# Optimization experiments

Hardware: AMD Instinct MI355X
Metric: run time of the kernel (lower is better)

The kernel has to match this reference:

```python
import jax, jax.numpy as jnp
import numpy as np

DIM, WIDTH = 5, 64
BATCH, N_SAVE = 4096, 64
RTOL, ATOL = 1e-3, 1e-6
SAFETY, FMIN, FMAX = 0.9, 0.2, 10.0
MAX_STEPS, DT0, EPS = 64, 0.1, 1e-6

# Tsit5 (Tsitouras 2011) Butcher tableau
A21 = 0.161
A31, A32 = -0.008480655492356989, 0.335480655492357
A41, A42, A43 = 2.8971530571054935, -6.359448489975075, 4.3622954328695815
A51, A52, A53, A54 = 5.325864828439257, -11.748883564062828, 7.4955393428898365, -0.09249506636175525
A61, A62, A63, A64, A65 = 5.86145544294642, -12.92096931784711, 8.159367898576159, -0.071584973281401, -0.028269050394068383
B1, B2, B3, B4, B5, B6 = 0.09646076681806523, 0.01, 0.4798896504144996, 1.379008574103742, -3.290069515436081, 2.324710524099774
# embedded 4th-order error coefficients (b - bhat)
E1, E2, E3, E4, E5, E6, E7 = (-0.00178001105222577714, -0.0008164344596567469,
    0.007880878010261995, -0.1447110071732629, 0.5823571654525552,
    -0.45808210592918697, 0.015151515151515152)


def _mlp(y, W1, b1, W2, b2, W3, b3, W4, b4):
    # eqx.nn.MLP(5, 5, width 64, depth 3, softplus)
    h = jax.nn.softplus(y @ W1.T + b1)
    h = jax.nn.softplus(h @ W2.T + b2)
    h = jax.nn.softplus(h @ W3.T + b3)
    return h @ W4.T + b4


def _solve_one(y0, t_eval, params):
    f = lambda y: _mlp(y, *params)
    t0, t1 = t_eval[0], t_eval[-1]
    # save points at/before t0 get y0
    ys0 = jnp.where((t_eval <= t0 + EPS)[:, None], y0[None, :], 0.0)

    def body(carry, _):
        t, y, h, ys = carry
        done = t >= t1 - EPS
        hc = jnp.where(done, 0.0, jnp.minimum(h, t1 - t))  # clip last step to t1
        k1 = f(y)
        k2 = f(y + hc * (A21 * k1))
        k3 = f(y + hc * (A31 * k1 + A32 * k2))
        k4 = f(y + hc * (A41 * k1 + A42 * k2 + A43 * k3))
        k5 = f(y + hc * (A51 * k1 + A52 * k2 + A53 * k3 + A54 * k4))
        k6 = f(y + hc * (A61 * k1 + A62 * k2 + A63 * k3 + A64 * k4 + A65 * k5))
        ynew = y + hc * (B1 * k1 + B2 * k2 + B3 * k3 + B4 * k4 + B5 * k5 + B6 * k6)
        k7 = f(ynew)  # FSAL stage, also used for error + interpolation
        err = hc * (E1 * k1 + E2 * k2 + E3 * k3 + E4 * k4 + E5 * k5 + E6 * k6 + E7 * k7)
        scale = ATOL + RTOL * jnp.maximum(jnp.abs(y), jnp.abs(ynew))
        enorm = jnp.sqrt(jnp.mean((err / scale) ** 2))
        enorm_c = jax.lax.stop_gradient(jnp.maximum(enorm, 1e-10))
        accept = enorm <= 1.0
        factor = jnp.clip(SAFETY * enorm_c ** -0.2, FMIN, FMAX)  # I-controller, order 5
        step_ok = accept & ~done
        t_next = jnp.where(step_ok, t + hc, t)
        y_next = jnp.where(step_ok, ynew, y)
        h_next = jnp.where(done, h, hc * factor)
        # cubic Hermite interpolation for save points inside (t, t_next]
        s = ((t_eval - t) / jnp.maximum(hc, 1e-12))[:, None]
        h00 = 2 * s**3 - 3 * s**2 + 1
        h10 = s**3 - 2 * s**2 + s
        h01 = -2 * s**3 + 3 * s**2
        h11 = s**3 - s**2
        yi = h00 * y + h10 * hc * k1 + h01 * ynew + h11 * hc * k7
        mask = (t_eval > t) & (t_eval <= t_next + EPS) & step_ok
        ys = jnp.where(mask[:, None], yi, ys)
        return (t_next, y_next, h_next, ys), None

    h0 = jnp.asarray(DT0, dtype=y0.dtype)
    (_, _, _, ys), _ = jax.lax.scan(body, (t0, y0, h0, ys0), None, length=MAX_STEPS)
    return ys  # [N_SAVE, DIM]


def setup_inputs() -> dict:
    key = jax.random.key(0)
    ks = jax.random.split(key, 9)
    y0 = jax.random.normal(ks[0], (BATCH, DIM), dtype=jnp.float32)
    t_eval = jnp.linspace(0.0, 1.0, N_SAVE, dtype=jnp.float32)

    def lin(k, out_d, in_d):
        lim = 1.0 / np.sqrt(in_d)
        kw, kb = jax.random.split(k)
        W = jax.random.uniform(kw, (out_d, in_d), jnp.float32, -lim, lim)
        b = jax.random.uniform(kb, (out_d,), jnp.float32, -lim, lim)
        return W, b

    W1, b1 = lin(ks[1], WIDTH, DIM)
    W2, b2 = lin(ks[2], WIDTH, WIDTH)
    W3, b3 = lin(ks[3], WIDTH, WIDTH)
    W4, b4 = lin(ks[4], DIM, WIDTH)
    return {"y0": y0, "t_eval": t_eval, "W1": W1, "b1": b1, "W2": W2, "b2": b2,
            "W3": W3, "b3": b3, "W4": W4, "b4": b4}


def reference(y0, t_eval, W1, b1, W2, b2, W3, b3, W4, b4):
    params = (W1, b1, W2, b2, W3, b3, W4, b4)
    return jax.vmap(lambda y: _solve_one(y, t_eval, params))(y0)  # [BATCH, N_SAVE, DIM]
```

## Files before the change

### kernel.cpp

```cpp
#include <hip/hip_runtime.h>
#include <cmath>

namespace {

constexpr int kDim = 5;
constexpr int kSave = 64;
constexpr int kTraj = 16;
constexpr int kThreads = 256;
constexpr int kMaxSteps = 64;
constexpr int HS = 72;
constexpr int SD = 8;

typedef _Float16 half8 __attribute__((ext_vector_type(8)));
typedef float f32x4 __attribute__((ext_vector_type(4)));

__device__ __forceinline__ float softplusf(float x) {
  return fmaxf(x, 0.0f) + __logf(1.0f + __expf(-fabsf(x)));
}

__global__ __launch_bounds__(kThreads, 1)
void node_tsit5_kernel(const float* __restrict__ gy0,
                       const float* __restrict__ gte,
                       const float* __restrict__ gW1, const float* __restrict__ gb1,
                       const float* __restrict__ gW2, const float* __restrict__ gb2,
                       const float* __restrict__ gW3, const float* __restrict__ gb3,
                       const float* __restrict__ gW4, const float* __restrict__ gb4,
                       float* __restrict__ out) {
  const float A21 = 0.161f;
  const float A31 = -0.008480655492356989f, A32 = 0.335480655492357f;
  const float A41 = 2.8971530571054935f, A42 = -6.359448489975075f, A43 = 4.3622954328695815f;
  const float A51 = 5.325864828439257f, A52 = -11.748883564062828f, A53 = 7.4955393428898365f,
              A54 = -0.09249506636175525f;
  const float A61 = 5.86145544294642f, A62 = -12.92096931784711f, A63 = 8.159367898576159f,
              A64 = -0.071584973281401f, A65 = -0.028269050394068383f;
  const float B1 = 0.09646076681806523f, B2 = 0.01f, B3 = 0.4798896504144996f,
              B4 = 1.379008574103742f, B5 = -3.290069515436081f, B6 = 2.324710524099774f;
  const float E1 = -0.00178001105222577714f, E2 = -0.0008164344596567469f,
              E3 = 0.007880878010261995f, E4 = -0.1447110071732629f, E5 = 0.5823571654525552f,
              E6 = -0.45808210592918697f, E7 = 0.015151515151515152f;

  __shared__ __align__(16) _Float16 h0[kTraj * HS], l0[kTraj * HS];
  __shared__ __align__(16) _Float16 h1[kTraj * HS], l1[kTraj * HS];
  __shared__ __align__(16) _Float16 h2[kTraj * HS], l2[kTraj * HS];
  __shared__ float sTe[kSave];
  __shared__ float sY[kTraj * SD], sYN[kTraj * SD], sK1[kTraj * SD], sK7[kTraj * SD];
  __shared__ float sesq[kTraj * SD];
  __shared__ float s_hc[kTraj], s_tOld[kTraj], s_tn[kTraj];
  __shared__ int s_ok[kTraj], s_done[kTraj];

  const int tid = threadIdx.x;
  const int bid = blockIdx.x;
  const int w = tid >> 6;
  const int ln = tid & 63;
  const int quad = ln >> 4;
  const int col = ln & 15;
  const int row0 = quad * 4;
  const int nn = (w << 4) | col;
  const bool cact = col < kDim;
  const bool w0 = (w == 0);

  half8 w2h[2], w3h[2], w4h[2], mfh[2];
  float w1r[kDim];
  #pragma unroll
  for (int d = 0; d < kDim; ++d) w1r[d] = gW1[nn * 5 + d];
  #pragma unroll
  for (int kf = 0; kf < 2; ++kf)
    #pragma unroll
    for (int j = 0; j < 8; ++j) {
      int kk2 = kf * 32 + quad * 8 + j;
      w2h[kf][j] = (_Float16)gW2[nn * 64 + kk2];
      w3h[kf][j] = (_Float16)gW3[nn * 64 + kk2];
      w4h[kf][j] = cact ? (_Float16)gW4[col * 64 + kk2] : (_Float16)0.0f;
      float m = 0.0f;
      #pragma unroll
      for (int d = 0; d < kDim; ++d) m = fmaf(w1r[d], gW4[d * 64 + kk2], m);
      mfh[kf][j] = (_Float16)m;
    }
  const float c1 = gb1[nn], c2 = gb2[nn], c3 = gb3[nn];
  const float c4 = cact ? gb4[col] : 0.0f;
  float cu = 0.0f;
  #pragma unroll
  for (int d = 0; d < kDim; ++d) cu = fmaf(w1r[d], gb4[d], cu);

  if (tid < kSave) sTe[tid] = gte[tid];
  if (tid < kTraj * kDim) {
    int t = tid & 15, d = tid >> 4;
    sY[t * SD + d] = gy0[(size_t)(bid * kTraj + t) * kDim + d];
  }
  {
    float* ob = out + (size_t)bid * kTraj * kSave * kDim;
    for (int idx = tid; idx < kTraj * kSave * kDim; idx += kThreads) ob[idx] = 0.0f;
  }

  f32x4 syr = {0, 0, 0, 0}, synr = {0, 0, 0, 0}, kk[7], uu[7], p_y;
  #pragma unroll
  for (int r = 0; r < 4; ++r) {
    const float* yr = gy0 + (size_t)(bid * kTraj + row0 + r) * kDim;
    float acc = c1;
    #pragma unroll
    for (int d = 0; d < kDim; ++d) acc = fmaf(w1r[d], yr[d], acc);
    p_y[r] = acc;
    if (cact) syr[r] = yr[col];
  }
  __syncthreads();

  const float t0v = sTe[0];
  const float t1v = sTe[kSave - 1];

  {
    int tt = tid & 15, gg = tid >> 4;
    float yv[kDim];
    #pragma unroll
    for (int d = 0; d < kDim; ++d) yv[d] = sY[tt * SD + d];
    #pragma unroll
    for (int q = 0; q < 4; ++q) {
      int n = 4 * gg + q;
      if (sTe[n] <= t0v + 1e-6f) {
        float* op = out + ((size_t)(bid * kTraj + tt) * kSave + n) * kDim;
        #pragma unroll
        for (int d = 0; d < kDim; ++d) op[d] = yv[d];
      }
    }
  }

  auto evalF = [&](f32x4 pre1, f32x4& kOut, f32x4& uOut) {
    #pragma unroll
    for (int r = 0; r < 4; ++r) {
      float s = softplusf(pre1[r]);
      _Float16 hi = (_Float16)s;
      h0[(row0 + r) * HS + nn] = hi;
      l0[(row0 + r) * HS + nn] = (_Float16)(s - (float)hi);
    }
    __syncthreads();
    {
      half8 ah0 = *(const half8*)(h0 + col * HS + quad * 8);
      half8 ah1 = *(const half8*)(h0 + col * HS + 32 + quad * 8);
      half8 al0 = *(const half8*)(l0 + col * HS + quad * 8);
      half8 al1 = *(const half8*)(l0 + col * HS + 32 + quad * 8);
      f32x4 a = {c2, c2, c2, c2};
      f32x4 b = {0, 0, 0, 0};
      a = __builtin_amdgcn_mfma_f32_16x16x32_f16(ah0, w2h[0], a, 0, 0, 0);
      b = __builtin_amdgcn_mfma_f32_16x16x32_f16(al0, w2h[0], b, 0, 0, 0);
      a = __builtin_amdgcn_mfma_f32_16x16x32_f16(ah1, w2h[1], a, 0, 0, 0);
      b = __builtin_amdgcn_mfma_f32_16x16x32_f16(al1, w2h[1], b, 0, 0, 0);
      a += b;
      #pragma unroll
      for (int r = 0; r < 4; ++r) {
        float s = softplusf(a[r]);
        _Float16 hi = (_Float16)s;
        h1[(row0 + r) * HS + nn] = hi;
        l1[(row0 + r) * HS + nn] = (_Float16)(s - (float)hi);
      }
    }
    __syncthreads();
    {
      half8 ah0 = *(const half8*)(h1 + col * HS + quad * 8);
      half8 ah1 = *(const half8*)(h1 + col * HS + 32 + quad * 8);
      half8 al0 = *(const half8*)(l1 + col * HS + quad * 8);
      half8 al1 = *(const half8*)(l1 + col * HS + 32 + quad * 8);
      f32x4 a = {c3, c3, c3, c3};
      f32x4 b = {0, 0, 0, 0};
      a = __builtin_amdgcn_mfma_f32_16x16x32_f16(ah0, w3h[0], a, 0, 0, 0);
      b = __builtin_amdgcn_mfma_f32_16x16x32_f16(al0, w3h[0], b, 0, 0, 0);
      a = __builtin_amdgcn_mfma_f32_16x16x32_f16(ah1, w3h[1], a, 0, 0, 0);
      b = __builtin_amdgcn_mfma_f32_16x16x32_f16(al1, w3h[1], b, 0, 0, 0);
      a += b;
      #pragma unroll
      for (int r = 0; r < 4; ++r) {
        float s = softplusf(a[r]);
        _Float16 hi = (_Float16)s;
        h2[(row0 + r) * HS + nn] = hi;
        l2[(row0 + r) * HS + nn] = (_Float16)(s - (float)hi);
      }
    }
    __syncthreads();
    {
      half8 ah0 = *(const half8*)(h2 + col * HS + quad * 8);
      half8 ah1 = *(const half8*)(h2 + col * HS + 32 + quad * 8);
      half8 al0 = *(const half8*)(l2 + col * HS + quad * 8);
      half8 al1 = *(const half8*)(l2 + col * HS + 32 + quad * 8);
      f32x4 ka = {c4, c4, c4, c4};
      f32x4 kb = {0, 0, 0, 0};
      f32x4 ua = {cu, cu, cu, cu};
      f32x4 ub = {0, 0, 0, 0};
      ka = __builtin_amdgcn_mfma_f32_16x16x32_f16(ah0, w4h[0], ka, 0, 0, 0);
      kb = __builtin_amdgcn_mfma_f32_16x16x32_f16(al0, w4h[0], kb, 0, 0, 0);
      ua = __builtin_amdgcn_mfma_f32_16x16x32_f16(ah0, mfh[0], ua, 0, 0, 0);
      ub = __builtin_amdgcn_mfma_f32_16x16x32_f16(al0, mfh[0], ub, 0, 0, 0);
      ka = __builtin_amdgcn_mfma_f32_16x16x32_f16(ah1, w4h[1], ka, 0, 0, 0);
      kb = __builtin_amdgcn_mfma_f32_16x16x32_f16(al1, w4h[1], kb, 0, 0, 0);
      ua = __builtin_amdgcn_mfma_f32_16x16x32_f16(ah1, mfh[1], ua, 0, 0, 0);
      ub = __builtin_amdgcn_mfma_f32_16x16x32_f16(al1, mfh[1], ub, 0, 0, 0);
      kOut = ka + kb;
      uOut = ua + ub;
    }
  };

  evalF(p_y, kk[0], uu[0]);

  float tcur = t0v, hcur = 0.1f;

  for (int step = 0; step < kMaxSteps; ++step) {
    if (ln < kTraj) {
      int dn = tcur >= t1v - 1e-6f;
      float hc = dn ? 0.0f : fminf(hcur, t1v - tcur);
      if (w0) { s_done[ln] = dn; s_hc[ln] = hc; s_tOld[ln] = tcur; }
    }
    __syncthreads();
    if (__ballot(s_done[ln & 15]) == ~0ull) break;

    f32x4 hcr;
    #pragma unroll
    for (int r = 0; r < 4; ++r) hcr[r] = s_hc[row0 + r];

    f32x4 p1;
    #pragma unroll
    for (int r = 0; r < 4; ++r) p1[r] = fmaf(hcr[r], A21 * uu[0][r], p_y[r]);
    evalF(p1, kk[1], uu[1]);

    #pragma unroll
    for (int r = 0; r < 4; ++r)
      p1[r] = fmaf(hcr[r], fmaf(A32, uu[1][r], A31 * uu[0][r]), p_y[r]);
    evalF(p1, kk[2], uu[2]);

    #pragma unroll
    for (int r = 0; r < 4; ++r)
      p1[r] = fmaf(hcr[r], fmaf(A43, uu[2][r], fmaf(A42, uu[1][r], A41 * uu[0][r])), p_y[r]);
    evalF(p1, kk[3], uu[3]);

    #pragma unroll
    for (int r = 0; r < 4; ++r)
      p1[r] = fmaf(hcr[r], fmaf(A54, uu[3][r], fmaf(A53, uu[2][r],
                  fmaf(A52, uu[1][r], A51 * uu[0][r]))), p_y[r]);
    evalF(p1, kk[4], uu[4]);

    #pragma unroll
    for (int r = 0; r < 4; ++r)
      p1[r] = fmaf(hcr[r], fmaf(A65, uu[4][r], fmaf(A64, uu[3][r], fmaf(A63, uu[2][r],
                  fmaf(A62, uu[1][r], A61 * uu[0][r])))), p_y[r]);
    evalF(p1, kk[5], uu[5]);

    f32x4 bu;
    #pragma unroll
    for (int r = 0; r < 4; ++r) {
      bu[r] = fmaf(B6, uu[5][r], fmaf(B5, uu[4][r], fmaf(B4, uu[3][r],
              fmaf(B3, uu[2][r], fmaf(B2, uu[1][r], B1 * uu[0][r])))));
      synr[r] = fmaf(hcr[r], fmaf(B6, kk[5][r], fmaf(B5, kk[4][r], fmaf(B4, kk[3][r],
                 fmaf(B3, kk[2][r], fmaf(B2, kk[1][r], B1 * kk[0][r]))))), syr[r]);
      p1[r] = fmaf(hcr[r], bu[r], p_y[r]);
    }
    evalF(p1, kk[6], uu[6]);

    if (w0 && cact) {
      #pragma unroll
      for (int r = 0; r < 4; ++r) {
        float err = hcr[r] * fmaf(E7, kk[6][r], fmaf(E6, kk[5][r], fmaf(E5, kk[4][r],
                    fmaf(E4, kk[3][r], fmaf(E3, kk[2][r], fmaf(E2, kk[1][r], E1 * kk[0][r]))))));
        float sc = fmaf(1e-3f, fmaxf(fabsf(syr[r]), fabsf(synr[r])), 1e-6f);
        float rr = err / sc;
        int o = (row0 + r) * SD + col;
        sesq[o] = rr * rr;
        sYN[o] = synr[r];
        sK1[o] = kk[0][r];
        sK7[o] = kk[6][r];
      }
    }
    __syncthreads();
    if (ln < kTraj) {
      float s = 0.0f;
      #pragma unroll
      for (int d = 0; d < kDim; ++d) s += sesq[ln * SD + d];
      float enorm = sqrtf(s / 5.0f);
      float enc = fmaxf(enorm, 1e-10f);
      int accept = enorm <= 1.0f;
      float factor = fminf(fmaxf(0.9f * powf(enc, -0.2f), 0.2f), 10.0f);
      int dn = s_done[ln];
      int ok = accept && !dn;
      float hc = s_hc[ln];
      float tn = ok ? tcur + hc : tcur;
      if (w0) { s_tn[ln] = tn; s_ok[ln] = ok; }
      tcur = tn;
      hcur = dn ? hcur : hc * factor;
    }
    __syncthreads();
    {
      int tt = tid & 15, gg = tid >> 4;
      if (s_ok[tt]) {
        float tOld = s_tOld[tt], hcs = s_hc[tt], tNew = s_tn[tt];
        float inv = 1.0f / fmaxf(hcs, 1e-12f);
        float yv[kDim], ynv[kDim], k1v[kDim], k7v[kDim];
        #pragma unroll
        for (int d = 0; d < kDim; ++d) {
          yv[d] = sY[tt * SD + d];
          ynv[d] = sYN[tt * SD + d];
          k1v[d] = hcs * sK1[tt * SD + d];
          k7v[d] = hcs * sK7[tt * SD + d];
        }
        #pragma unroll
        for (int q = 0; q < 4; ++q) {
          int n = 4 * gg + q;
          float te = sTe[n];
          if (te > tOld && te <= tNew + 1e-6f) {
            float sx = (te - tOld) * inv;
            float s2 = sx * sx, s3 = s2 * sx;
            float h00 = 2.f * s3 - 3.f * s2 + 1.f;
            float h10 = s3 - 2.f * s2 + sx;
            float h01 = -2.f * s3 + 3.f * s2;
            float h11 = s3 - s2;
            float* op = out + ((size_t)(bid * kTraj + tt) * kSave + n) * kDim;
            #pragma unroll
            for (int d = 0; d < kDim; ++d)
              op[d] = h00 * yv[d] + h10 * k1v[d] + h01 * ynv[d] + h11 * k7v[d];
          }
        }
      }
    }
    __syncthreads();
    #pragma unroll
    for (int r = 0; r < 4; ++r) {
      int ok = s_ok[row0 + r];
      if (ok) {
        syr[r] = synr[r];
        kk[0][r] = kk[6][r];
        uu[0][r] = uu[6][r];
        p_y[r] = fmaf(hcr[r], bu[r], p_y[r]);
      }
      if (w0 && cact) sY[(row0 + r) * SD + col] = syr[r];
    }
    __syncthreads();
  }
}

}

extern "C" void kernel_launch(void* const* d_in, const int* in_sizes, int n_in,
                              void* d_out, int out_size, void* d_ws, size_t ws_size,
                              hipStream_t stream) {
  const float* y0 = (const float*)d_in[0];
  const float* te = (const float*)d_in[1];
  const float* W1 = (const float*)d_in[2];
  const float* b1 = (const float*)d_in[3];
  const float* W2 = (const float*)d_in[4];
  const float* b2 = (const float*)d_in[5];
  const float* W3 = (const float*)d_in[6];
  const float* b3 = (const float*)d_in[7];
  const float* W4 = (const float*)d_in[8];
  const float* b4 = (const float*)d_in[9];
  float* out = (float*)d_out;

  const int batch = in_sizes[0] / kDim;
  const int blocks = batch / kTraj;
  hipLaunchKernelGGL(node_tsit5_kernel, dim3(blocks), dim3(kThreads), 0, stream,
                     y0, te, W1, b1, W2, b2, W3, b3, W4, b4, out);
}
```

Baseline: 107.8 us.

## Compute step control per wave with shuffles and drop block barriers

Each lane now keeps its own copy of time, step size and done flags in registers. The error norm is reduced with wave-level xor shuffles instead of a shared-memory pass by one group of lanes. This removes three of the four __syncthreads per step and the shared control arrays, leaving only one barrier before dense-output interpolation. powf is also replaced by fast exp/log. The main risk is shared-memory hazards on sY/sYN/sK1/ct* across iterations, which now rely on barriers inside evalF; the fast exp/log also changes step-size rounding slightly.

```diff
diff --git a/kernel.cpp b/kernel.cpp
--- a/kernel.cpp
+++ b/kernel.cpp
@@ -44,9 +44,7 @@
   __shared__ __align__(16) _Float16 h2[kTraj * HS], l2[kTraj * HS];
   __shared__ float sTe[kSave];
   __shared__ float sY[kTraj * SD], sYN[kTraj * SD], sK1[kTraj * SD], sK7[kTraj * SD];
-  __shared__ float sesq[kTraj * SD];
-  __shared__ float s_hc[kTraj], s_tOld[kTraj], s_tn[kTraj];
-  __shared__ int s_ok[kTraj], s_done[kTraj];
+  __shared__ float ctT[kTraj], ctH[kTraj], ctN[kTraj], ctO[kTraj];
 
   const int tid = threadIdx.x;
   const int bid = blockIdx.x;
@@ -198,45 +196,47 @@
 
   evalF(p_y, kk[0], uu[0]);
 
-  float tcur = t0v, hcur = 0.1f;
+  f32x4 tcur = {t0v, t0v, t0v, t0v};
+  f32x4 hcur = {0.1f, 0.1f, 0.1f, 0.1f};
 
   for (int step = 0; step < kMaxSteps; ++step) {
-    if (ln < kTraj) {
-      int dn = tcur >= t1v - 1e-6f;
-      float hc = dn ? 0.0f : fminf(hcur, t1v - tcur);
-      if (w0) { s_done[ln] = dn; s_hc[ln] = hc; s_tOld[ln] = tcur; }
-    }
-    __syncthreads();
-    if (__ballot(s_done[ln & 15]) == ~0ull) break;
-
-    f32x4 hcr;
-    #pragma unroll
-    for (int r = 0; r < 4; ++r) hcr[r] = s_hc[row0 + r];
+    f32x4 hcs, tOldr;
+    bool dnr[4];
+    bool all4 = true;
+    #pragma unroll
+    for (int r = 0; r < 4; ++r) {
+      bool d = tcur[r] >= t1v - 1e-6f;
+      dnr[r] = d;
+      all4 &= d;
+      hcs[r] = d ? 0.0f : fminf(hcur[r], t1v - tcur[r]);
+      tOldr[r] = tcur[r];
+    }
+    if (__ballot(all4) == ~0ull) break;
 
     f32x4 p1;
     #pragma unroll
-    for (int r = 0; r < 4; ++r) p1[r] = fmaf(hcr[r], A21 * uu[0][r], p_y[r]);
+    for (int r = 0; r < 4; ++r) p1[r] = fmaf(hcs[r], A21 * uu[0][r], p_y[r]);
     evalF(p1, kk[1], uu[1]);
 
     #pragma unroll
     for (int r = 0; r < 4; ++r)
-      p1[r] = fmaf(hcr[r], fmaf(A32, uu[1][r], A31 * uu[0][r]), p_y[r]);
+      p1[r] = fmaf(hcs[r], fmaf(A32, uu[1][r], A31 * uu[0][r]), p_y[r]);
     evalF(p1, kk[2], uu[2]);
 
     #pragma unroll
     for (int r = 0; r < 4; ++r)
-      p1[r] = fmaf(hcr[r], fmaf(A43, uu[2][r], fmaf(A42, uu[1][r], A41 * uu[0][r])), p_y[r]);
+      p1[r] = fmaf(hcs[r], fmaf(A43, uu[2][r], fmaf(A42, uu[1][r], A41 * uu[0][r])), p_y[r]);
     evalF(p1, kk[3], uu[3]);
 
     #pragma unroll
     for (int r = 0; r < 4; ++r)
-      p1[r] = fmaf(hcr[r], fmaf(A54, uu[3][r], fmaf(A53, uu[2][r],
+      p1[r] = fmaf(hcs[r], fmaf(A54, uu[3][r], fmaf(A53, uu[2][r],
                   fmaf(A52, uu[1][r], A51 * uu[0][r]))), p_y[r]);
     evalF(p1, kk[4], uu[4]);
 
     #pragma unroll
     for (int r = 0; r < 4; ++r)
-      p1[r] = fmaf(hcr[r], fmaf(A65, uu[4][r], fmaf(A64, uu[3][r], fmaf(A63, uu[2][r],
+      p1[r] = fmaf(hcs[r], fmaf(A65, uu[4][r], fmaf(A64, uu[3][r], fmaf(A63, uu[2][r],
                   fmaf(A62, uu[1][r], A61 * uu[0][r])))), p_y[r]);
     evalF(p1, kk[5], uu[5]);
 
@@ -245,56 +245,77 @@
     for (int r = 0; r < 4; ++r) {
       bu[r] = fmaf(B6, uu[5][r], fmaf(B5, uu[4][r], fmaf(B4, uu[3][r],
               fmaf(B3, uu[2][r], fmaf(B2, uu[1][r], B1 * uu[0][r])))));
-      synr[r] = fmaf(hcr[r], fmaf(B6, kk[5][r], fmaf(B5, kk[4][r], fmaf(B4, kk[3][r],
+      synr[r] = fmaf(hcs[r], fmaf(B6, kk[5][r], fmaf(B5, kk[4][r], fmaf(B4, kk[3][r],
                  fmaf(B3, kk[2][r], fmaf(B2, kk[1][r], B1 * kk[0][r]))))), syr[r]);
-      p1[r] = fmaf(hcr[r], bu[r], p_y[r]);
-    }
-    evalF(p1, kk[6], uu[6]);
-
+      p1[r] = fmaf(hcs[r], bu[r], p_y[r]);
+    }
     if (w0 && cact) {
       #pragma unroll
       for (int r = 0; r < 4; ++r) {
-        float err = hcr[r] * fmaf(E7, kk[6][r], fmaf(E6, kk[5][r], fmaf(E5, kk[4][r],
-                    fmaf(E4, kk[3][r], fmaf(E3, kk[2][r], fmaf(E2, kk[1][r], E1 * kk[0][r]))))));
-        float sc = fmaf(1e-3f, fmaxf(fabsf(syr[r]), fabsf(synr[r])), 1e-6f);
-        float rr = err / sc;
         int o = (row0 + r) * SD + col;
-        sesq[o] = rr * rr;
+        sY[o] = syr[r];
         sYN[o] = synr[r];
         sK1[o] = kk[0][r];
-        sK7[o] = kk[6][r];
+      }
+    }
+    evalF(p1, kk[6], uu[6]);
+
+    f32x4 rr2;
+    #pragma unroll
+    for (int r = 0; r < 4; ++r) {
+      float err = hcs[r] * fmaf(E7, kk[6][r], fmaf(E6, kk[5][r], fmaf(E5, kk[4][r],
+                  fmaf(E4, kk[3][r], fmaf(E3, kk[2][r], fmaf(E2, kk[1][r], E1 * kk[0][r]))))));
+      float sc = fmaf(1e-3f, fmaxf(fabsf(syr[r]), fabsf(synr[r])), 1e-6f);
+      float rr = err / sc;
+      rr2[r] = cact ? rr * rr : 0.0f;
+    }
+    #pragma unroll
+    for (int m = 1; m < 16; m <<= 1) {
+      #pragma unroll
+      for (int r = 0; r < 4; ++r) rr2[r] += __shfl_xor(rr2[r], m, 64);
+    }
+
+    bool okr[4];
+    #pragma unroll
+    for (int r = 0; r < 4; ++r) {
+      float enorm = sqrtf(rr2[r] / 5.0f);
+      float enc = fmaxf(enorm, 1e-10f);
+      bool accept = enorm <= 1.0f;
+      float factor = fminf(fmaxf(0.9f * __expf(-0.2f * __logf(enc)), 0.2f), 10.0f);
+      bool ok = accept && !dnr[r];
+      okr[r] = ok;
+      tcur[r] = ok ? tcur[r] + hcs[r] : tcur[r];
+      hcur[r] = dnr[r] ? hcur[r] : hcs[r] * factor;
+    }
+
+    if (w0 && cact) {
+      #pragma unroll
+      for (int r = 0; r < 4; ++r) sK7[(row0 + r) * SD + col] = kk[6][r];
+    }
+    if (w0 && col == 0) {
+      #pragma unroll
+      for (int r = 0; r < 4; ++r) {
+        int m2 = row0 + r;
+        ctT[m2] = tOldr[r];
+        ctH[m2] = hcs[r];
+        ctN[m2] = tcur[r];
+        ctO[m2] = okr[r] ? 1.0f : 0.0f;
       }
     }
     __syncthreads();
-    if (ln < kTraj) {
-      float s = 0.0f;
-      #pragma unroll
-      for (int d = 0; d < kDim; ++d) s += sesq[ln * SD + d];
-      float enorm = sqrtf(s / 5.0f);
-      float enc = fmaxf(enorm, 1e-10f);
-      int accept = enorm <= 1.0f;
-      float factor = fminf(fmaxf(0.9f * powf(enc, -0.2f), 0.2f), 10.0f);
-      int dn = s_done[ln];
-      int ok = accept && !dn;
-      float hc = s_hc[ln];
-      float tn = ok ? tcur + hc : tcur;
-      if (w0) { s_tn[ln] = tn; s_ok[ln] = ok; }
-      tcur = tn;
-      hcur = dn ? hcur : hc * factor;
-    }
-    __syncthreads();
+
     {
       int tt = tid & 15, gg = tid >> 4;
-      if (s_ok[tt]) {
-        float tOld = s_tOld[tt], hcs = s_hc[tt], tNew = s_tn[tt];
-        float inv = 1.0f / fmaxf(hcs, 1e-12f);
+      if (ctO[tt] != 0.0f) {
+        float tOld = ctT[tt], hcv = ctH[tt], tNew = ctN[tt];
+        float inv = 1.0f / fmaxf(hcv, 1e-12f);
         float yv[kDim], ynv[kDim], k1v[kDim], k7v[kDim];
         #pragma unroll
         for (int d = 0; d < kDim; ++d) {
           yv[d] = sY[tt * SD + d];
           ynv[d] = sYN[tt * SD + d];
-          k1v[d] = hcs * sK1[tt * SD + d];
-          k7v[d] = hcs * sK7[tt * SD + d];
+          k1v[d] = hcv * sK1[tt * SD + d];
+          k7v[d] = hcv * sK7[tt * SD + d];
         }
         #pragma unroll
         for (int q = 0; q < 4; ++q) {
@@ -315,19 +336,16 @@
         }
       }
     }
-    __syncthreads();
-    #pragma unroll
-    for (int r = 0; r < 4; ++r) {
-      int ok = s_ok[row0 + r];
-      if (ok) {
+
+    #pragma unroll
+    for (int r = 0; r < 4; ++r) {
+      if (okr[r]) {
         syr[r] = synr[r];
         kk[0][r] = kk[6][r];
         uu[0][r] = uu[6][r];
-        p_y[r] = fmaf(hcr[r], bu[r], p_y[r]);
-      }
-      if (w0 && cact) sY[(row0 + r) * SD + col] = syr[r];
-    }
-    __syncthreads();
+        p_y[r] = fmaf(hcs[r], bu[r], p_y[r]);
+      }
+    }
   }
 }
 
```

New measurement: 107.8 us. Within noise of the previous version (+0.1%).
